# Optimization experiments

Measured on AMD Instinct MI355X. Metric: run time of the kernel, lower is better.

## Reference

```python
import jax, jax.numpy as jnp
import numpy as np

NUM_HEAD = 8
NUM_BOX = 4
K = 4                      # kernel_size
P = K * K                  # num_point
HEAD_DIM = 32
V_DIM = 256
Q_DIM = 256


def _kernel_indices():
    # even kernel: linspace(-K/2+0.5, K/2-0.5, K), stack (j, i) i.e. (x, y), /K
    idx = np.linspace(-K // 2 + 0.5, K // 2 - 0.5, K)
    i, j = np.meshgrid(idx, idx, indexing='ij')
    return jnp.asarray(np.stack([j, i], axis=-1).reshape(-1, 2) / K, dtype=jnp.float32)


def _bilinear(vm, gx, gy, Hf, Wf):
    # vm: [b,H,Hf*Wf,dh]; gx,gy: [b,H,M] normalized coords in [0,1]
    # grid_sample(2*g-1, align_corners=False, padding_mode='zeros') semantics
    x = gx * Wf - 0.5
    y = gy * Hf - 0.5
    x0 = jnp.floor(x)
    y0 = jnp.floor(y)
    wx1 = x - x0
    wy1 = y - y0

    def corner(xi, yi, w):
        inb = (xi >= 0) & (xi < Wf) & (yi >= 0) & (yi < Hf)
        xi_c = jnp.clip(xi, 0, Wf - 1).astype(jnp.int32)
        yi_c = jnp.clip(yi, 0, Hf - 1).astype(jnp.int32)
        v = jnp.take_along_axis(vm, (yi_c * Wf + xi_c)[..., None], axis=2)
        return v * (w * inb)[..., None]

    return (corner(x0, y0, (1 - wx1) * (1 - wy1))
            + corner(x0 + 1, y0, wx1 * (1 - wy1))
            + corner(x0, y0 + 1, (1 - wx1) * wy1)
            + corner(x0 + 1, y0 + 1, wx1 * wy1))


def _forward(query, value, Hf, Wf, v_mask, v_valid_ratios, ref_windows,
             box_w, box_b, attn_w, attn_b, vproj_w, vproj_b, oproj_w, oproj_b):
    b, l1, _ = query.shape
    l2 = value.shape[1]
    ki = _kernel_indices()  # [P,2]

    value = value @ vproj_w.T + vproj_b
    value = jnp.where(v_mask[..., None], 0.0, value)
    vm = value.reshape(b, l2, NUM_HEAD, HEAD_DIM).transpose(0, 2, 1, 3)  # [b,H,l2,dh]

    off = (query @ box_w.T + box_b).reshape(b, l1, NUM_HEAD, NUM_BOX, 4)
    ref = ref_windows[:, :, None, None, :]                   # [b,l1,1,1,4]
    ref_size = ref[..., jnp.array([2, 3, 2, 3])]
    boxes = ref + off / 8.0 * ref_size                       # [b,l1,H,B,4]
    center = boxes[..., None, :2]
    size = boxes[..., None, 2:]
    grid = center + ki * jax.nn.relu(size)                   # [b,l1,H,B,P,2]
    grid = grid * v_valid_ratios

    # attention weights: [b,l1,H,B,2,2] -> repeat_interleave -> [b,l1,H,B,K,K]
    aw = (query @ attn_w.T + attn_b).reshape(b, l1, NUM_HEAD, NUM_BOX, 2, 2)
    aw = jnp.repeat(jnp.repeat(aw, K // 2, axis=-1), K // 2, axis=-2)
    spatial_w = jax.nn.softmax(aw.reshape(b, l1, NUM_HEAD, NUM_BOX * P), axis=-1)
    level_w = jax.nn.softmax(aw, axis=3).reshape(b, l1, NUM_HEAD, NUM_BOX * P)

    # per-head bilinear sampling at all B*P points per query
    g = grid.transpose(0, 2, 1, 3, 4, 5).reshape(b, NUM_HEAD, -1, 2)  # [b,H,l1*B*P,2]
    sampled = _bilinear(vm, g[..., 0], g[..., 1], Hf, Wf)             # [b,H,M,dh]
    sampled = sampled.reshape(b, NUM_HEAD, l1, NUM_BOX * P, HEAD_DIM)

    out = jnp.einsum('bhlpd,blhp->blhd', sampled, spatial_w).reshape(b, l1, V_DIM)
    output = out @ oproj_w.T + oproj_b
    # mask branch: level softmax (over boxes) weighted aggregate, summed over points
    mout = jnp.einsum('bhlpd,blhp->blhd', sampled, level_w).reshape(b, l1, V_DIM)
    mask_output = mout @ oproj_w.T + oproj_b
    return output, mask_output, aw


def setup_inputs() -> dict:
    key = jax.random.key(0)
    ks = jax.random.split(key, 12)
    b, l1, Hf, Wf = 8, 300, 64, 64
    l2 = Hf * Wf
    d = Q_DIM
    return {
        'query': jax.random.normal(ks[0], (b, l1, d), jnp.float32),
        'value': jax.random.normal(ks[1], (b, l2, V_DIM), jnp.float32),
        'v_shape': np.array([[Hf, Wf]], dtype=np.int64),
        'v_mask': jnp.zeros((b, l2), dtype=bool),
        'v_start_index': np.array([0], dtype=np.int64),
        'v_valid_ratios': jnp.ones((b, 1, 1, 1, 1, 2), jnp.float32),
        'ref_windows': jax.random.uniform(ks[2], (b, l1, 4), jnp.float32, 0.05, 0.6),
        'box_w': 0.02 * jax.random.normal(ks[3], (NUM_BOX * NUM_HEAD * 4, d), jnp.float32),
        'box_b': jax.random.uniform(ks[4], (NUM_HEAD * NUM_BOX * 4,), jnp.float32),
        'attn_w': 0.02 * jax.random.normal(ks[5], (NUM_HEAD * NUM_BOX * 4, d), jnp.float32),
        'attn_b': 0.1 * jax.random.normal(ks[6], (NUM_HEAD * NUM_BOX * 4,), jnp.float32),
        'vproj_w': 0.05 * jax.random.normal(ks[7], (V_DIM, V_DIM), jnp.float32),
        'vproj_b': jnp.zeros((V_DIM,), jnp.float32),
        'oproj_w': 0.05 * jax.random.normal(ks[8], (d, V_DIM), jnp.float32),
        'oproj_b': jnp.zeros((d,), jnp.float32),
    }


def reference(query, value, v_shape, v_mask, v_start_index, v_valid_ratios, ref_windows,
              box_w, box_b, attn_w, attn_b, vproj_w, vproj_b, oproj_w, oproj_b):
    Hf, Wf = int(v_shape[0, 0]), int(v_shape[0, 1])  # single level, static shapes
    return _forward(query, value, Hf, Wf, v_mask, v_valid_ratios, ref_windows,
                    box_w, box_b, attn_w, attn_b, vproj_w, vproj_b, oproj_w, oproj_b)
```

## Files before the change

kernel.cpp:

```cpp
#include <hip/hip_runtime.h>
#include <cstddef>

#define NH   8
#define NB   4
#define HD   32
#define NPIX 4096
#define NBATCH 8
#define NL   300
#define D    256
#define NQ   (NBATCH * NL)
#define NR   (2 * NQ)

typedef __attribute__((ext_vector_type(4))) float  f32x4;
typedef __attribute__((ext_vector_type(8))) short  bf16x8;

__device__ __forceinline__ unsigned short f2bf(float f) {
    union { float f; unsigned u; } v; v.f = f;
    unsigned r = v.u + 0x7fffu + ((v.u >> 16) & 1u);
    return (unsigned short)(r >> 16);
}
__device__ __forceinline__ float bf2f(unsigned short u) {
    union { unsigned u; float f; } v; v.u = ((unsigned)u) << 16; return v.f;
}
__device__ __forceinline__ unsigned cvtpk(float lo, float hi) {
    unsigned r;
    asm("v_cvt_pk_bf16_f32 %0, %1, %2" : "=v"(r) : "v"(lo), "v"(hi));
    return r;
}
__device__ __forceinline__ bf16x8 pack8c(f32x4 a, f32x4 b) {
    union { unsigned u[4]; bf16x8 v; } r;
    r.u[0] = cvtpk(a[0], a[1]); r.u[1] = cvtpk(a[2], a[3]);
    r.u[2] = cvtpk(b[0], b[1]); r.u[3] = cvtpk(b[2], b[3]);
    return r.v;
}

__global__ __launch_bounds__(256)
void tow_kernel(const float* __restrict__ vproj_w, const float* __restrict__ oproj_w,
                unsigned short* __restrict__ wv, unsigned short* __restrict__ wo)
{
    const int i = blockIdx.x * 256 + threadIdx.x;
    const float* src = (i < 8192) ? vproj_w : oproj_w;
    unsigned short* dst = (i < 8192) ? wv : wo;
    const size_t off = (size_t)(i & 8191) * 8;
    f32x4 a = *(const f32x4*)(src + off);
    f32x4 b = *(const f32x4*)(src + off + 4);
    *(bf16x8*)(dst + off) = pack8c(a, b);
}

__global__ __launch_bounds__(256)
void fat_kernel(const float* __restrict__ value, const unsigned short* __restrict__ Wv,
                const float* __restrict__ vbias, const unsigned char* __restrict__ mask,
                unsigned short* __restrict__ vm,
                const float* __restrict__ query,
                const float* __restrict__ box_w, const float* __restrict__ box_b,
                const float* __restrict__ attn_w, const float* __restrict__ attn_b,
                float* __restrict__ bp, float* __restrict__ ap, float* __restrict__ awo)
{
    __shared__ float As[16][65];
    __shared__ float Bs[16][65];
    const int bid = blockIdx.x;
    const int tid = threadIdx.x;

    if (bid < 512) {
        const int lane = tid & 63, wid = tid >> 6;
        const int wm = wid >> 1, wn = wid & 1;
        const int row0 = bid * 64;
        const int l16 = lane & 15, lg = lane >> 4;

        f32x4 acc[2][8] = {};
        const float*          pa0 = value + (size_t)(row0 + wm * 32 + l16) * D + lg * 8;
        const unsigned short* pb0 = Wv    + (size_t)(wn * 128 + l16) * D + lg * 8;

        #pragma unroll
        for (int ks = 0; ks < 8; ++ks) {
            bf16x8 af[2], bfr[8];
            #pragma unroll
            for (int m = 0; m < 2; ++m) {
                const float* pa = pa0 + (size_t)m * 16 * D + ks * 32;
                af[m] = pack8c(*(const f32x4*)pa, *(const f32x4*)(pa + 4));
            }
            #pragma unroll
            for (int n = 0; n < 8; ++n)
                bfr[n] = *(const bf16x8*)(pb0 + (size_t)n * 16 * D + ks * 32);
            #pragma unroll
            for (int m = 0; m < 2; ++m)
                #pragma unroll
                for (int n = 0; n < 8; ++n)
                    acc[m][n] = __builtin_amdgcn_mfma_f32_16x16x32_bf16(af[m], bfr[n], acc[m][n], 0, 0, 0);
        }
        #pragma unroll
        for (int m = 0; m < 2; ++m) {
            #pragma unroll
            for (int r = 0; r < 4; ++r) {
                const int grow = row0 + wm * 32 + m * 16 + lg * 4 + r;
                const int bb = grow >> 12, pix = grow & (NPIX - 1);
                const float mf = (mask[grow] != 0) ? 0.f : 1.f;
                #pragma unroll
                for (int n = 0; n < 8; ++n) {
                    const int gcol = wn * 128 + n * 16 + l16;
                    const int h = gcol >> 5, dd = gcol & 31;
                    vm[((size_t)(bb * NH + h) * NPIX + pix) * HD + dd] =
                        f2bf(mf * (acc[m][n][r] + vbias[gcol]));
                }
            }
        }
    } else {
        const int pid = bid - 512;
        const int row0 = (pid % 38) * 64, col0 = (pid / 38) * 64;
        const int tr = tid >> 4, tc = tid & 15;
        float acc[4][4] = {};
        for (int k0 = 0; k0 < D; k0 += 16) {
            #pragma unroll
            for (int i = 0; i < 4; ++i) {
                int idx = tid + i * 256;
                int r = idx >> 4, kk = idx & 15;
                int qrow = min(row0 + r, NQ - 1);
                As[kk][r] = query[(size_t)qrow * D + k0 + kk];
                int c256 = col0 + r;
                const float* src = (c256 < 128) ? (box_w + (size_t)c256 * D)
                                                : (attn_w + (size_t)(c256 - 128) * D);
                Bs[kk][r] = src[k0 + kk];
            }
            __syncthreads();
            #pragma unroll
            for (int kk = 0; kk < 16; ++kk) {
                float a[4], bv[4];
                #pragma unroll
                for (int i = 0; i < 4; ++i) a[i] = As[kk][tr * 4 + i];
                #pragma unroll
                for (int j = 0; j < 4; ++j) bv[j] = Bs[kk][tc * 4 + j];
                #pragma unroll
                for (int i = 0; i < 4; ++i)
                    #pragma unroll
                    for (int j = 0; j < 4; ++j)
                        acc[i][j] += a[i] * bv[j];
            }
            __syncthreads();
        }
        #pragma unroll
        for (int i = 0; i < 4; ++i) {
            int q = row0 + tr * 4 + i;
            if (q >= NQ) continue;
            #pragma unroll
            for (int j = 0; j < 4; ++j) {
                int col = col0 + tc * 4 + j;
                if (col < 128) {
                    bp[(size_t)q * 128 + col] = acc[i][j] + box_b[col];
                } else {
                    int rc = col - 128;
                    float val = acc[i][j] + attn_b[rc];
                    ap[(size_t)q * 128 + rc] = val;
                    int h = rc >> 4, bx = (rc >> 2) & 3, rr = (rc >> 1) & 1, cc = rc & 1;
                    float* awq = awo + (size_t)q * 512 + (size_t)(h * NB + bx) * 16;
                    awq[(2 * rr + 0) * 4 + 2 * cc + 0] = val;
                    awq[(2 * rr + 0) * 4 + 2 * cc + 1] = val;
                    awq[(2 * rr + 1) * 4 + 2 * cc + 0] = val;
                    awq[(2 * rr + 1) * 4 + 2 * cc + 1] = val;
                }
            }
        }
    }
}

__global__ __launch_bounds__(256)
void sample_kernel(const unsigned short* __restrict__ vm, const float* __restrict__ bp,
                   const float* __restrict__ ap, const float* __restrict__ ref_windows,
                   const float* __restrict__ vratio, const int* __restrict__ vshape,
                   float* __restrict__ outp, float* __restrict__ moutp)
{
    __shared__ float sbp[128], sap[128], swh[128], lwh[128], sref4[4];
    __shared__ float4 boxdat[32];
    __shared__ int4   O4[512];
    __shared__ float4 W4[512];
    __shared__ float2 SL[512];
    const int blk = blockIdx.x, tid = threadIdx.x;
    const int bb = blk / NL;
    if (tid < 128) { sbp[tid] = bp[(size_t)blk * 128 + tid]; sap[tid] = ap[(size_t)blk * 128 + tid]; }
    if (tid < 4) sref4[tid] = ref_windows[(size_t)blk * 4 + tid];
    __syncthreads();
    const int Hf = vshape[0], Wf = vshape[1];
    const float Hff = (float)Hf, Wff = (float)Wf;
    const float vr0 = vratio[bb * 2 + 0], vr1 = vratio[bb * 2 + 1];

    if (tid < 128) {
        float a = sap[tid];
        float m = a;
        m = fmaxf(m, __shfl_xor(m, 1));
        m = fmaxf(m, __shfl_xor(m, 2));
        m = fmaxf(m, __shfl_xor(m, 4));
        m = fmaxf(m, __shfl_xor(m, 8));
        float e = expf(a - m);
        float ldv = e + __shfl_xor(e, 4);
        ldv += __shfl_xor(ldv, 8);
        float ss = ldv + __shfl_xor(ldv, 1);
        ss += __shfl_xor(ss, 2);
        swh[tid] = e / (4.f * ss);
        lwh[tid] = e / ldv;
    } else if (tid < 160) {
        int j = tid - 128;
        float o0 = sbp[j * 4 + 0], o1 = sbp[j * 4 + 1];
        float o2 = sbp[j * 4 + 2], o3 = sbp[j * 4 + 3];
        float cx = sref4[0] + o0 * 0.125f * sref4[2];
        float cy = sref4[1] + o1 * 0.125f * sref4[3];
        float rw = fmaxf(sref4[2] + o2 * 0.125f * sref4[2], 0.f);
        float rh = fmaxf(sref4[3] + o3 * 0.125f * sref4[3], 0.f);
        boxdat[j] = make_float4(cx, cy, rw, rh);
    }
    __syncthreads();

    const float kidx[4] = {-0.375f, -0.125f, 0.125f, 0.375f};
    #pragma unroll
    for (int pp = 0; pp < 2; ++pp) {
        const int p = tid + pp * 256;
        const float4 bd = boxdat[p >> 4];
        const int ii = (p >> 2) & 3, jj = p & 3;
        const float gy = (bd.y + kidx[ii] * bd.w) * vr1;
        const float gx = (bd.x + kidx[jj] * bd.z) * vr0;
        const float y = gy * Hff - 0.5f, x = gx * Wff - 0.5f;
        const float y0f = floorf(y), x0f = floorf(x);
        const int iy0 = (int)y0f, ix0 = (int)x0f;
        const float wy1 = y - y0f, wx1 = x - x0f;
        const float wy0 = 1.f - wy1, wx0 = 1.f - wx1;
        const bool y0in = (iy0 >= 0) & (iy0 < Hf);
        const bool y1in = (iy0 + 1 >= 0) & (iy0 + 1 < Hf);
        const bool x0in = (ix0 >= 0) & (ix0 < Wf);
        const bool x1in = (ix0 + 1 >= 0) & (ix0 + 1 < Wf);
        const int yc0 = min(max(iy0, 0), Hf - 1), yc1 = min(max(iy0 + 1, 0), Hf - 1);
        const int xc0 = min(max(ix0, 0), Wf - 1), xc1 = min(max(ix0 + 1, 0), Wf - 1);
        O4[p] = make_int4((yc0 * Wf + xc0) * HD, (yc0 * Wf + xc1) * HD,
                          (yc1 * Wf + xc0) * HD, (yc1 * Wf + xc1) * HD);
        W4[p] = make_float4((y0in & x0in) ? wy0 * wx0 : 0.f,
                            (y0in & x1in) ? wy0 * wx1 : 0.f,
                            (y1in & x0in) ? wy1 * wx0 : 0.f,
                            (y1in & x1in) ? wy1 * wx1 : 0.f);
        const int kpos = ((p >> 2) & 2) | ((p >> 1) & 1);
        const int hk = (p >> 6) * 16 + ((p >> 4) & 3) * 4 + kpos;
        SL[p] = make_float2(swh[hk], lwh[hk]);
    }
    __syncthreads();

    const int h = tid >> 5, dd = tid & 31;
    const unsigned short* base = vm + ((size_t)(bb * NH + h) * NPIX) * HD + dd;
    float acc = 0.f, accm = 0.f;
    #pragma unroll 4
    for (int t = 0; t < 64; ++t) {
        const int p = h * 64 + t;
        const int4 o = O4[p]; const float4 w = W4[p]; const float2 sl = SL[p];
        const float samp = bf2f(base[o.x]) * w.x + bf2f(base[o.y]) * w.y
                         + bf2f(base[o.z]) * w.z + bf2f(base[o.w]) * w.w;
        acc  += samp * sl.x;
        accm += samp * sl.y;
    }
    outp[(size_t)blk * 256 + tid]  = acc;
    moutp[(size_t)blk * 256 + tid] = accm;
}

__global__ __launch_bounds__(256)
void oproj_direct(const float* __restrict__ R, const unsigned short* __restrict__ Wo,
                  const float* __restrict__ bias, float* __restrict__ Out)
{
    const int tid  = threadIdx.x;
    const int lane = tid & 63, wid = tid >> 6;
    const int wm = wid >> 1, wn = wid & 1;
    const int row0 = blockIdx.x * 64;
    const int l16 = lane & 15, lg = lane >> 4;

    f32x4 acc[2][8] = {};
    const float*          pa0 = R  + (size_t)(row0 + wm * 32 + l16) * D + lg * 8;
    const unsigned short* pb0 = Wo + (size_t)(wn * 128 + l16) * D + lg * 8;

    #pragma unroll
    for (int ks = 0; ks < 8; ++ks) {
        bf16x8 af[2], bfr[8];
        #pragma unroll
        for (int m = 0; m < 2; ++m) {
            const float* pa = pa0 + (size_t)m * 16 * D + ks * 32;
            af[m] = pack8c(*(const f32x4*)pa, *(const f32x4*)(pa + 4));
        }
        #pragma unroll
        for (int n = 0; n < 8; ++n)
            bfr[n] = *(const bf16x8*)(pb0 + (size_t)n * 16 * D + ks * 32);
        #pragma unroll
        for (int m = 0; m < 2; ++m)
            #pragma unroll
            for (int n = 0; n < 8; ++n)
                acc[m][n] = __builtin_amdgcn_mfma_f32_16x16x32_bf16(af[m], bfr[n], acc[m][n], 0, 0, 0);
    }
    #pragma unroll
    for (int m = 0; m < 2; ++m) {
        #pragma unroll
        for (int r = 0; r < 4; ++r) {
            const int grow = row0 + wm * 32 + m * 16 + lg * 4 + r;
            #pragma unroll
            for (int n = 0; n < 8; ++n) {
                const int gcol = wn * 128 + n * 16 + l16;
                Out[(size_t)grow * D + gcol] = acc[m][n][r] + bias[gcol];
            }
        }
    }
}

extern "C" void kernel_launch(void* const* d_in, const int* in_sizes, int n_in,
                              void* d_out, int out_size, void* d_ws, size_t ws_size,
                              hipStream_t stream)
{
    const float* query        = (const float*)d_in[0];
    const float* value        = (const float*)d_in[1];
    const int*   vshape       = (const int*)d_in[2];
    const unsigned char* vmask= (const unsigned char*)d_in[3];
    const float* vratio       = (const float*)d_in[5];
    const float* refw         = (const float*)d_in[6];
    const float* box_w        = (const float*)d_in[7];
    const float* box_b        = (const float*)d_in[8];
    const float* attn_w       = (const float*)d_in[9];
    const float* attn_b       = (const float*)d_in[10];
    const float* vproj_w      = (const float*)d_in[11];
    const float* vproj_b      = (const float*)d_in[12];
    const float* oproj_w      = (const float*)d_in[13];
    const float* oproj_b      = (const float*)d_in[14];

    unsigned short* vm_b = (unsigned short*)d_ws;
    unsigned short* wv   = vm_b + 8388608;
    unsigned short* wo   = wv + 65536;
    float* bp = (float*)(wo + 65536);
    float* ap = bp + 307200;

    float* out1 = (float*)d_out;
    float* out2 = out1 + 614400;
    float* awo  = out2 + 614400;

    float* outp  = out1;
    float* moutp = out2;

    tow_kernel<<<64, 256, 0, stream>>>(vproj_w, oproj_w, wv, wo);
    fat_kernel<<<664, 256, 0, stream>>>(value, wv, vproj_b, vmask, vm_b,
                                        query, box_w, box_b, attn_w, attn_b, bp, ap, awo);
    sample_kernel<<<NQ, 256, 0, stream>>>(vm_b, bp, ap, refw, vratio, vshape, outp, moutp);
    oproj_direct<<<75, 256, 0, stream>>>(out1, wo, oproj_b, out1);
}
```

Measured before the change: 206.7 us.

## Stage GEMM operands in LDS with bf16 conversion and drop weight pre-conversion kernel

The value-projection and output-projection GEMMs now load fp32 tiles from global memory, convert them to bf16, and stage them in shared memory before the MFMA loops. Previously each wave read its operands straight from global memory. Operands are now reused across waves and the separate weight-conversion kernel launch is removed. The output projection moves to 128x256 tiles on 512-thread blocks, which halves the block count to 38. That may underuse the GPU's compute units, and the GEMMs now pay for extra barriers and shared-memory traffic.

```diff
diff --git a/kernel.cpp b/kernel.cpp
--- a/kernel.cpp
+++ b/kernel.cpp
@@ -35,20 +35,7 @@
 }
 
 __global__ __launch_bounds__(256)
-void tow_kernel(const float* __restrict__ vproj_w, const float* __restrict__ oproj_w,
-                unsigned short* __restrict__ wv, unsigned short* __restrict__ wo)
-{
-    const int i = blockIdx.x * 256 + threadIdx.x;
-    const float* src = (i < 8192) ? vproj_w : oproj_w;
-    unsigned short* dst = (i < 8192) ? wv : wo;
-    const size_t off = (size_t)(i & 8191) * 8;
-    f32x4 a = *(const f32x4*)(src + off);
-    f32x4 b = *(const f32x4*)(src + off + 4);
-    *(bf16x8*)(dst + off) = pack8c(a, b);
-}
-
-__global__ __launch_bounds__(256)
-void fat_kernel(const float* __restrict__ value, const unsigned short* __restrict__ Wv,
+void fat_kernel(const float* __restrict__ value, const float* __restrict__ Wvf,
                 const float* __restrict__ vbias, const unsigned char* __restrict__ mask,
                 unsigned short* __restrict__ vm,
                 const float* __restrict__ query,
@@ -56,48 +43,57 @@
                 const float* __restrict__ attn_w, const float* __restrict__ attn_b,
                 float* __restrict__ bp, float* __restrict__ ap, float* __restrict__ awo)
 {
-    __shared__ float As[16][65];
-    __shared__ float Bs[16][65];
+    __shared__ __align__(16) short As[128][72];
+    __shared__ __align__(16) short Bs[128][72];
     const int bid = blockIdx.x;
     const int tid = threadIdx.x;
 
     if (bid < 512) {
+        const int mt = bid >> 1, nt = bid & 1;
+        const int row0 = mt * 128, col0 = nt * 128;
         const int lane = tid & 63, wid = tid >> 6;
         const int wm = wid >> 1, wn = wid & 1;
-        const int row0 = bid * 64;
         const int l16 = lane & 15, lg = lane >> 4;
 
-        f32x4 acc[2][8] = {};
-        const float*          pa0 = value + (size_t)(row0 + wm * 32 + l16) * D + lg * 8;
-        const unsigned short* pb0 = Wv    + (size_t)(wn * 128 + l16) * D + lg * 8;
-
-        #pragma unroll
-        for (int ks = 0; ks < 8; ++ks) {
-            bf16x8 af[2], bfr[8];
-            #pragma unroll
-            for (int m = 0; m < 2; ++m) {
-                const float* pa = pa0 + (size_t)m * 16 * D + ks * 32;
-                af[m] = pack8c(*(const f32x4*)pa, *(const f32x4*)(pa + 4));
-            }
-            #pragma unroll
-            for (int n = 0; n < 8; ++n)
-                bfr[n] = *(const bf16x8*)(pb0 + (size_t)n * 16 * D + ks * 32);
-            #pragma unroll
-            for (int m = 0; m < 2; ++m)
-                #pragma unroll
-                for (int n = 0; n < 8; ++n)
-                    acc[m][n] = __builtin_amdgcn_mfma_f32_16x16x32_bf16(af[m], bfr[n], acc[m][n], 0, 0, 0);
-        }
-        #pragma unroll
-        for (int m = 0; m < 2; ++m) {
+        f32x4 acc[4][4] = {};
+        for (int k0 = 0; k0 < D; k0 += 64) {
+            #pragma unroll
+            for (int i = 0; i < 4; ++i) {
+                const int t = tid + i * 256;
+                const int r = t >> 3, c8 = (t & 7) * 8;
+                const float* p = value + (size_t)(row0 + r) * D + k0 + c8;
+                *(bf16x8*)&As[r][c8] = pack8c(*(const f32x4*)p, *(const f32x4*)(p + 4));
+                const float* q = Wvf + (size_t)(col0 + r) * D + k0 + c8;
+                *(bf16x8*)&Bs[r][c8] = pack8c(*(const f32x4*)q, *(const f32x4*)(q + 4));
+            }
+            __syncthreads();
+            #pragma unroll
+            for (int kk = 0; kk < 2; ++kk) {
+                bf16x8 af[4], bfr[4];
+                #pragma unroll
+                for (int m = 0; m < 4; ++m)
+                    af[m] = *(const bf16x8*)&As[wm * 64 + m * 16 + l16][kk * 32 + lg * 8];
+                #pragma unroll
+                for (int n = 0; n < 4; ++n)
+                    bfr[n] = *(const bf16x8*)&Bs[wn * 64 + n * 16 + l16][kk * 32 + lg * 8];
+                #pragma unroll
+                for (int m = 0; m < 4; ++m)
+                    #pragma unroll
+                    for (int n = 0; n < 4; ++n)
+                        acc[m][n] = __builtin_amdgcn_mfma_f32_16x16x32_bf16(af[m], bfr[n], acc[m][n], 0, 0, 0);
+            }
+            __syncthreads();
+        }
+        #pragma unroll
+        for (int m = 0; m < 4; ++m) {
             #pragma unroll
             for (int r = 0; r < 4; ++r) {
-                const int grow = row0 + wm * 32 + m * 16 + lg * 4 + r;
+                const int grow = row0 + wm * 64 + m * 16 + lg * 4 + r;
                 const int bb = grow >> 12, pix = grow & (NPIX - 1);
                 const float mf = (mask[grow] != 0) ? 0.f : 1.f;
                 #pragma unroll
-                for (int n = 0; n < 8; ++n) {
-                    const int gcol = wn * 128 + n * 16 + l16;
+                for (int n = 0; n < 4; ++n) {
+                    const int gcol = col0 + wn * 64 + n * 16 + l16;
                     const int h = gcol >> 5, dd = gcol & 31;
                     vm[((size_t)(bb * NH + h) * NPIX + pix) * HD + dd] =
                         f2bf(mf * (acc[m][n][r] + vbias[gcol]));
@@ -105,6 +101,8 @@
             }
         }
     } else {
+        float (*Asf)[65] = (float (*)[65])&As[0][0];
+        float (*Bsf)[65] = (float (*)[65])&Bs[0][0];
         const int pid = bid - 512;
         const int row0 = (pid % 38) * 64, col0 = (pid / 38) * 64;
         const int tr = tid >> 4, tc = tid & 15;
@@ -115,20 +113,20 @@
                 int idx = tid + i * 256;
                 int r = idx >> 4, kk = idx & 15;
                 int qrow = min(row0 + r, NQ - 1);
-                As[kk][r] = query[(size_t)qrow * D + k0 + kk];
+                Asf[kk][r] = query[(size_t)qrow * D + k0 + kk];
                 int c256 = col0 + r;
                 const float* src = (c256 < 128) ? (box_w + (size_t)c256 * D)
                                                 : (attn_w + (size_t)(c256 - 128) * D);
-                Bs[kk][r] = src[k0 + kk];
+                Bsf[kk][r] = src[k0 + kk];
             }
             __syncthreads();
             #pragma unroll
             for (int kk = 0; kk < 16; ++kk) {
                 float a[4], bv[4];
                 #pragma unroll
-                for (int i = 0; i < 4; ++i) a[i] = As[kk][tr * 4 + i];
-                #pragma unroll
-                for (int j = 0; j < 4; ++j) bv[j] = Bs[kk][tc * 4 + j];
+                for (int i = 0; i < 4; ++i) a[i] = Asf[kk][tr * 4 + i];
+                #pragma unroll
+                for (int j = 0; j < 4; ++j) bv[j] = Bsf[kk][tc * 4 + j];
                 #pragma unroll
                 for (int i = 0; i < 4; ++i)
                     #pragma unroll
@@ -255,45 +253,62 @@
     moutp[(size_t)blk * 256 + tid] = accm;
 }
 
-__global__ __launch_bounds__(256)
-void oproj_direct(const float* __restrict__ R, const unsigned short* __restrict__ Wo,
-                  const float* __restrict__ bias, float* __restrict__ Out)
+__global__ __launch_bounds__(512)
+void oproj_lds(const float* __restrict__ R, const float* __restrict__ Wof,
+               const float* __restrict__ bias, float* __restrict__ Out)
 {
+    __shared__ __align__(16) short As[128][72];
+    __shared__ __align__(16) short Bs[256][72];
     const int tid  = threadIdx.x;
     const int lane = tid & 63, wid = tid >> 6;
-    const int wm = wid >> 1, wn = wid & 1;
-    const int row0 = blockIdx.x * 64;
+    const int wm = wid >> 2, wn = wid & 3;
+    const int row0 = blockIdx.x * 128;
     const int l16 = lane & 15, lg = lane >> 4;
 
-    f32x4 acc[2][8] = {};
-    const float*          pa0 = R  + (size_t)(row0 + wm * 32 + l16) * D + lg * 8;
-    const unsigned short* pb0 = Wo + (size_t)(wn * 128 + l16) * D + lg * 8;
-
+    f32x4 acc[4][4] = {};
+    for (int k0 = 0; k0 < D; k0 += 64) {
+        #pragma unroll
+        for (int i = 0; i < 2; ++i) {
+            const int t = tid + i * 512;
+            const int r = t >> 3, c8 = (t & 7) * 8;
+            const int arow = min(row0 + r, NR - 1);
+            const float* p = R + (size_t)arow * D + k0 + c8;
+            *(bf16x8*)&As[r][c8] = pack8c(*(const f32x4*)p, *(const f32x4*)(p + 4));
+        }
+        #pragma unroll
+        for (int i = 0; i < 4; ++i) {
+            const int t = tid + i * 512;
+            const int r = t >> 3, c8 = (t & 7) * 8;
+            const float* q = Wof + (size_t)r * D + k0 + c8;
+            *(bf16x8*)&Bs[r][c8] = pack8c(*(const f32x4*)q, *(const f32x4*)(q + 4));
+        }
+        __syncthreads();
+        #pragma unroll
+        for (int kk = 0; kk < 2; ++kk) {
+            bf16x8 af[4], bfr[4];
+            #pragma unroll
+            for (int m = 0; m < 4; ++m)
+                af[m] = *(const bf16x8*)&As[wm * 64 + m * 16 + l16][kk * 32 + lg * 8];
+            #pragma unroll
+            for (int n = 0; n < 4; ++n)
+                bfr[n] = *(const bf16x8*)&Bs[wn * 64 + n * 16 + l16][kk * 32 + lg * 8];
+            #pragma unroll
+            for (int m = 0; m < 4; ++m)
+                #pragma unroll
+                for (int n = 0; n < 4; ++n)
+                    acc[m][n] = __builtin_amdgcn_mfma_f32_16x16x32_bf16(af[m], bfr[n], acc[m][n], 0, 0, 0);
+        }
+        __syncthreads();
+    }
     #pragma unroll
-    for (int ks = 0; ks < 8; ++ks) {
-        bf16x8 af[2], bfr[8];
-        #pragma unroll
-        for (int m = 0; m < 2; ++m) {
-            const float* pa = pa0 + (size_t)m * 16 * D + ks * 32;
-            af[m] = pack8c(*(const f32x4*)pa, *(const f32x4*)(pa + 4));
-        }
-        #pragma unroll
-        for (int n = 0; n < 8; ++n)
-            bfr[n] = *(const bf16x8*)(pb0 + (size_t)n * 16 * D + ks * 32);
-        #pragma unroll
-        for (int m = 0; m < 2; ++m)
-            #pragma unroll
-            for (int n = 0; n < 8; ++n)
-                acc[m][n] = __builtin_amdgcn_mfma_f32_16x16x32_bf16(af[m], bfr[n], acc[m][n], 0, 0, 0);
-    }
-    #pragma unroll
-    for (int m = 0; m < 2; ++m) {
+    for (int m = 0; m < 4; ++m) {
         #pragma unroll
         for (int r = 0; r < 4; ++r) {
-            const int grow = row0 + wm * 32 + m * 16 + lg * 4 + r;
-            #pragma unroll
-            for (int n = 0; n < 8; ++n) {
-                const int gcol = wn * 128 + n * 16 + l16;
+            const int grow = row0 + wm * 64 + m * 16 + lg * 4 + r;
+            if (grow >= NR) continue;
+            #pragma unroll
+            for (int n = 0; n < 4; ++n) {
+                const int gcol = wn * 64 + n * 16 + l16;
                 Out[(size_t)grow * D + gcol] = acc[m][n][r] + bias[gcol];
             }
         }
@@ -320,9 +335,7 @@
     const float* oproj_b      = (const float*)d_in[14];
 
     unsigned short* vm_b = (unsigned short*)d_ws;
-    unsigned short* wv   = vm_b + 8388608;
-    unsigned short* wo   = wv + 65536;
-    float* bp = (float*)(wo + 65536);
+    float* bp = (float*)(vm_b + 8388608);
     float* ap = bp + 307200;
 
     float* out1 = (float*)d_out;
@@ -332,9 +345,8 @@
     float* outp  = out1;
     float* moutp = out2;
 
-    tow_kernel<<<64, 256, 0, stream>>>(vproj_w, oproj_w, wv, wo);
-    fat_kernel<<<664, 256, 0, stream>>>(value, wv, vproj_b, vmask, vm_b,
+    fat_kernel<<<664, 256, 0, stream>>>(value, vproj_w, vproj_b, vmask, vm_b,
                                         query, box_w, box_b, attn_w, attn_b, bp, ap, awo);
     sample_kernel<<<NQ, 256, 0, stream>>>(vm_b, bp, ap, refw, vratio, vshape, outp, moutp);
-    oproj_direct<<<75, 256, 0, stream>>>(out1, wo, oproj_b, out1);
-}
+    oproj_lds<<<38, 512, 0, stream>>>(out1, oproj_w, oproj_b, out1);
+}
```

Result: faster. 198.0 us (-4.2%).

## Fuse output projection into sampling kernel and tile value projection through LDS

Applied to the files above, without the earlier changes.

The output projection is folded into the sampling kernel: each block keeps its two 256-wide sampled vectors in shared memory and runs a per-thread fp32 GEMV against the fp32 oproj weights. This removes the separate oproj GEMM launch and the global round trip of the intermediate. The value projection becomes its own 512-thread MFMA kernel that stages bf16-converted value and weight tiles in LDS with register prefetch, which drops the weight-conversion pre-kernel. The query projection is split out as a separate 2D-grid kernel, and sample blocks are remapped to interleave batches. The cost is that every sampling block re-reads the full fp32 oproj weight with strided per-thread row loads, does that GEMV without tensor cores, and the two projection GEMMs no longer share one launch.

```diff
diff --git a/kernel.cpp b/kernel.cpp
--- a/kernel.cpp
+++ b/kernel.cpp
@@ -9,7 +9,6 @@
 #define NL   300
 #define D    256
 #define NQ   (NBATCH * NL)
-#define NR   (2 * NQ)
 
 typedef __attribute__((ext_vector_type(4))) float  f32x4;
 typedef __attribute__((ext_vector_type(8))) short  bf16x8;
@@ -34,129 +33,137 @@
     return r.v;
 }
 
+__global__ __launch_bounds__(512, 4)
+void vproj_kernel(const float* __restrict__ value, const float* __restrict__ Wvf,
+                  const float* __restrict__ vbias, const unsigned char* __restrict__ mask,
+                  unsigned short* __restrict__ vm)
+{
+    __shared__ __align__(16) short As[64][72];
+    __shared__ __align__(16) short Bs[256][72];
+    const int tid  = threadIdx.x;
+    const int lane = tid & 63, wid = tid >> 6;
+    const int wm = wid >> 2, wn = wid & 3;
+    const int row0 = blockIdx.x * 64;
+    const int l16 = lane & 15, lg = lane >> 4;
+
+    const int sr = tid >> 3, sc8 = (tid & 7) * 8;
+
+    f32x4 acc[2][4] = {};
+    f32x4 pA[2], pB[8];
+
+    auto LOADK = [&](int k0) {
+        const float* p = value + (size_t)(row0 + sr) * D + k0 + sc8;
+        pA[0] = *(const f32x4*)p; pA[1] = *(const f32x4*)(p + 4);
+        #pragma unroll
+        for (int i = 0; i < 4; ++i) {
+            const float* q = Wvf + (size_t)(sr + i * 64) * D + k0 + sc8;
+            pB[2 * i] = *(const f32x4*)q; pB[2 * i + 1] = *(const f32x4*)(q + 4);
+        }
+    };
+
+    LOADK(0);
+    #pragma unroll
+    for (int ks = 0; ks < 4; ++ks) {
+        *(bf16x8*)&As[sr][sc8] = pack8c(pA[0], pA[1]);
+        #pragma unroll
+        for (int i = 0; i < 4; ++i)
+            *(bf16x8*)&Bs[sr + i * 64][sc8] = pack8c(pB[2 * i], pB[2 * i + 1]);
+        __syncthreads();
+        if (ks < 3) LOADK((ks + 1) * 64);
+        #pragma unroll
+        for (int kk = 0; kk < 2; ++kk) {
+            bf16x8 af[2], bfr[4];
+            #pragma unroll
+            for (int m = 0; m < 2; ++m)
+                af[m] = *(const bf16x8*)&As[wm * 32 + m * 16 + l16][kk * 32 + lg * 8];
+            #pragma unroll
+            for (int n = 0; n < 4; ++n)
+                bfr[n] = *(const bf16x8*)&Bs[wn * 64 + n * 16 + l16][kk * 32 + lg * 8];
+            #pragma unroll
+            for (int m = 0; m < 2; ++m)
+                #pragma unroll
+                for (int n = 0; n < 4; ++n)
+                    acc[m][n] = __builtin_amdgcn_mfma_f32_16x16x32_bf16(af[m], bfr[n], acc[m][n], 0, 0, 0);
+        }
+        __syncthreads();
+    }
+    #pragma unroll
+    for (int m = 0; m < 2; ++m) {
+        #pragma unroll
+        for (int r = 0; r < 4; ++r) {
+            const int grow = row0 + wm * 32 + m * 16 + lg * 4 + r;
+            const int bb = grow >> 12, pix = grow & (NPIX - 1);
+            const float mf = (mask[grow] != 0) ? 0.f : 1.f;
+            #pragma unroll
+            for (int n = 0; n < 4; ++n) {
+                const int gcol = wn * 64 + n * 16 + l16;
+                const int h = gcol >> 5, dd = gcol & 31;
+                vm[((size_t)(bb * NH + h) * NPIX + pix) * HD + dd] =
+                    f2bf(mf * (acc[m][n][r] + vbias[gcol]));
+            }
+        }
+    }
+}
+
 __global__ __launch_bounds__(256)
-void tow_kernel(const float* __restrict__ vproj_w, const float* __restrict__ oproj_w,
-                unsigned short* __restrict__ wv, unsigned short* __restrict__ wo)
-{
-    const int i = blockIdx.x * 256 + threadIdx.x;
-    const float* src = (i < 8192) ? vproj_w : oproj_w;
-    unsigned short* dst = (i < 8192) ? wv : wo;
-    const size_t off = (size_t)(i & 8191) * 8;
-    f32x4 a = *(const f32x4*)(src + off);
-    f32x4 b = *(const f32x4*)(src + off + 4);
-    *(bf16x8*)(dst + off) = pack8c(a, b);
-}
-
-__global__ __launch_bounds__(256)
-void fat_kernel(const float* __restrict__ value, const unsigned short* __restrict__ Wv,
-                const float* __restrict__ vbias, const unsigned char* __restrict__ mask,
-                unsigned short* __restrict__ vm,
-                const float* __restrict__ query,
-                const float* __restrict__ box_w, const float* __restrict__ box_b,
-                const float* __restrict__ attn_w, const float* __restrict__ attn_b,
-                float* __restrict__ bp, float* __restrict__ ap, float* __restrict__ awo)
+void proj_kernel(const float* __restrict__ query,
+                 const float* __restrict__ box_w, const float* __restrict__ box_b,
+                 const float* __restrict__ attn_w, const float* __restrict__ attn_b,
+                 float* __restrict__ bp, float* __restrict__ ap, float* __restrict__ awo)
 {
     __shared__ float As[16][65];
     __shared__ float Bs[16][65];
-    const int bid = blockIdx.x;
     const int tid = threadIdx.x;
-
-    if (bid < 512) {
-        const int lane = tid & 63, wid = tid >> 6;
-        const int wm = wid >> 1, wn = wid & 1;
-        const int row0 = bid * 64;
-        const int l16 = lane & 15, lg = lane >> 4;
-
-        f32x4 acc[2][8] = {};
-        const float*          pa0 = value + (size_t)(row0 + wm * 32 + l16) * D + lg * 8;
-        const unsigned short* pb0 = Wv    + (size_t)(wn * 128 + l16) * D + lg * 8;
-
-        #pragma unroll
-        for (int ks = 0; ks < 8; ++ks) {
-            bf16x8 af[2], bfr[8];
-            #pragma unroll
-            for (int m = 0; m < 2; ++m) {
-                const float* pa = pa0 + (size_t)m * 16 * D + ks * 32;
-                af[m] = pack8c(*(const f32x4*)pa, *(const f32x4*)(pa + 4));
-            }
-            #pragma unroll
-            for (int n = 0; n < 8; ++n)
-                bfr[n] = *(const bf16x8*)(pb0 + (size_t)n * 16 * D + ks * 32);
-            #pragma unroll
-            for (int m = 0; m < 2; ++m)
+    const int tr = tid >> 4, tc = tid & 15;
+    float acc[4][4] = {};
+    const int row0 = blockIdx.x * 64, col0 = blockIdx.y * 64;
+    for (int k0 = 0; k0 < D; k0 += 16) {
+        #pragma unroll
+        for (int i = 0; i < 4; ++i) {
+            int idx = tid + i * 256;
+            int r = idx >> 4, kk = idx & 15;
+            int qrow = min(row0 + r, NQ - 1);
+            As[kk][r] = query[(size_t)qrow * D + k0 + kk];
+            int c256 = col0 + r;
+            const float* src = (c256 < 128) ? (box_w + (size_t)c256 * D)
+                                            : (attn_w + (size_t)(c256 - 128) * D);
+            Bs[kk][r] = src[k0 + kk];
+        }
+        __syncthreads();
+        #pragma unroll
+        for (int kk = 0; kk < 16; ++kk) {
+            float a[4], bv[4];
+            #pragma unroll
+            for (int i = 0; i < 4; ++i) a[i] = As[kk][tr * 4 + i];
+            #pragma unroll
+            for (int j = 0; j < 4; ++j) bv[j] = Bs[kk][tc * 4 + j];
+            #pragma unroll
+            for (int i = 0; i < 4; ++i)
                 #pragma unroll
-                for (int n = 0; n < 8; ++n)
-                    acc[m][n] = __builtin_amdgcn_mfma_f32_16x16x32_bf16(af[m], bfr[n], acc[m][n], 0, 0, 0);
-        }
-        #pragma unroll
-        for (int m = 0; m < 2; ++m) {
-            #pragma unroll
-            for (int r = 0; r < 4; ++r) {
-                const int grow = row0 + wm * 32 + m * 16 + lg * 4 + r;
-                const int bb = grow >> 12, pix = grow & (NPIX - 1);
-                const float mf = (mask[grow] != 0) ? 0.f : 1.f;
-                #pragma unroll
-                for (int n = 0; n < 8; ++n) {
-                    const int gcol = wn * 128 + n * 16 + l16;
-                    const int h = gcol >> 5, dd = gcol & 31;
-                    vm[((size_t)(bb * NH + h) * NPIX + pix) * HD + dd] =
-                        f2bf(mf * (acc[m][n][r] + vbias[gcol]));
-                }
-            }
-        }
-    } else {
-        const int pid = bid - 512;
-        const int row0 = (pid % 38) * 64, col0 = (pid / 38) * 64;
-        const int tr = tid >> 4, tc = tid & 15;
-        float acc[4][4] = {};
-        for (int k0 = 0; k0 < D; k0 += 16) {
-            #pragma unroll
-            for (int i = 0; i < 4; ++i) {
-                int idx = tid + i * 256;
-                int r = idx >> 4, kk = idx & 15;
-                int qrow = min(row0 + r, NQ - 1);
-                As[kk][r] = query[(size_t)qrow * D + k0 + kk];
-                int c256 = col0 + r;
-                const float* src = (c256 < 128) ? (box_w + (size_t)c256 * D)
-                                                : (attn_w + (size_t)(c256 - 128) * D);
-                Bs[kk][r] = src[k0 + kk];
-            }
-            __syncthreads();
-            #pragma unroll
-            for (int kk = 0; kk < 16; ++kk) {
-                float a[4], bv[4];
-                #pragma unroll
-                for (int i = 0; i < 4; ++i) a[i] = As[kk][tr * 4 + i];
-                #pragma unroll
-                for (int j = 0; j < 4; ++j) bv[j] = Bs[kk][tc * 4 + j];
-                #pragma unroll
-                for (int i = 0; i < 4; ++i)
-                    #pragma unroll
-                    for (int j = 0; j < 4; ++j)
-                        acc[i][j] += a[i] * bv[j];
-            }
-            __syncthreads();
-        }
-        #pragma unroll
-        for (int i = 0; i < 4; ++i) {
-            int q = row0 + tr * 4 + i;
-            if (q >= NQ) continue;
-            #pragma unroll
-            for (int j = 0; j < 4; ++j) {
-                int col = col0 + tc * 4 + j;
-                if (col < 128) {
-                    bp[(size_t)q * 128 + col] = acc[i][j] + box_b[col];
-                } else {
-                    int rc = col - 128;
-                    float val = acc[i][j] + attn_b[rc];
-                    ap[(size_t)q * 128 + rc] = val;
-                    int h = rc >> 4, bx = (rc >> 2) & 3, rr = (rc >> 1) & 1, cc = rc & 1;
-                    float* awq = awo + (size_t)q * 512 + (size_t)(h * NB + bx) * 16;
-                    awq[(2 * rr + 0) * 4 + 2 * cc + 0] = val;
-                    awq[(2 * rr + 0) * 4 + 2 * cc + 1] = val;
-                    awq[(2 * rr + 1) * 4 + 2 * cc + 0] = val;
-                    awq[(2 * rr + 1) * 4 + 2 * cc + 1] = val;
-                }
+                for (int j = 0; j < 4; ++j)
+                    acc[i][j] += a[i] * bv[j];
+        }
+        __syncthreads();
+    }
+    #pragma unroll
+    for (int i = 0; i < 4; ++i) {
+        int q = row0 + tr * 4 + i;
+        if (q >= NQ) continue;
+        #pragma unroll
+        for (int j = 0; j < 4; ++j) {
+            int col = col0 + tc * 4 + j;
+            if (col < 128) {
+                bp[(size_t)q * 128 + col] = acc[i][j] + box_b[col];
+            } else {
+                int rc = col - 128;
+                float val = acc[i][j] + attn_b[rc];
+                ap[(size_t)q * 128 + rc] = val;
+                int h = rc >> 4, bx = (rc >> 2) & 3, rr = (rc >> 1) & 1, cc = rc & 1;
+                float* awq = awo + (size_t)q * 512 + (size_t)(h * NB + bx) * 16;
+                awq[(2 * rr + 0) * 4 + 2 * cc + 0] = val;
+                awq[(2 * rr + 0) * 4 + 2 * cc + 1] = val;
+                awq[(2 * rr + 1) * 4 + 2 * cc + 0] = val;
+                awq[(2 * rr + 1) * 4 + 2 * cc + 1] = val;
             }
         }
     }
@@ -166,14 +173,17 @@
 void sample_kernel(const unsigned short* __restrict__ vm, const float* __restrict__ bp,
                    const float* __restrict__ ap, const float* __restrict__ ref_windows,
                    const float* __restrict__ vratio, const int* __restrict__ vshape,
-                   float* __restrict__ outp, float* __restrict__ moutp)
+                   const float* __restrict__ oproj_w, const float* __restrict__ oproj_b,
+                   float* __restrict__ out1, float* __restrict__ out2)
 {
     __shared__ float sbp[128], sap[128], swh[128], lwh[128], sref4[4];
     __shared__ float4 boxdat[32];
     __shared__ int4   O4[512];
     __shared__ float4 W4[512];
     __shared__ float2 SL[512];
-    const int blk = blockIdx.x, tid = threadIdx.x;
+    __shared__ __align__(16) float r1s[256], r2s[256];
+    const int bid = blockIdx.x, tid = threadIdx.x;
+    const int blk = (bid & 7) * NL + (bid >> 3);
     const int bb = blk / NL;
     if (tid < 128) { sbp[tid] = bp[(size_t)blk * 128 + tid]; sap[tid] = ap[(size_t)blk * 128 + tid]; }
     if (tid < 4) sref4[tid] = ref_windows[(size_t)blk * 4 + tid];
@@ -239,65 +249,36 @@
     }
     __syncthreads();
 
-    const int h = tid >> 5, dd = tid & 31;
-    const unsigned short* base = vm + ((size_t)(bb * NH + h) * NPIX) * HD + dd;
-    float acc = 0.f, accm = 0.f;
-    #pragma unroll 4
-    for (int t = 0; t < 64; ++t) {
-        const int p = h * 64 + t;
-        const int4 o = O4[p]; const float4 w = W4[p]; const float2 sl = SL[p];
-        const float samp = bf2f(base[o.x]) * w.x + bf2f(base[o.y]) * w.y
-                         + bf2f(base[o.z]) * w.z + bf2f(base[o.w]) * w.w;
-        acc  += samp * sl.x;
-        accm += samp * sl.y;
-    }
-    outp[(size_t)blk * 256 + tid]  = acc;
-    moutp[(size_t)blk * 256 + tid] = accm;
-}
-
-__global__ __launch_bounds__(256)
-void oproj_direct(const float* __restrict__ R, const unsigned short* __restrict__ Wo,
-                  const float* __restrict__ bias, float* __restrict__ Out)
-{
-    const int tid  = threadIdx.x;
-    const int lane = tid & 63, wid = tid >> 6;
-    const int wm = wid >> 1, wn = wid & 1;
-    const int row0 = blockIdx.x * 64;
-    const int l16 = lane & 15, lg = lane >> 4;
-
-    f32x4 acc[2][8] = {};
-    const float*          pa0 = R  + (size_t)(row0 + wm * 32 + l16) * D + lg * 8;
-    const unsigned short* pb0 = Wo + (size_t)(wn * 128 + l16) * D + lg * 8;
-
-    #pragma unroll
-    for (int ks = 0; ks < 8; ++ks) {
-        bf16x8 af[2], bfr[8];
-        #pragma unroll
-        for (int m = 0; m < 2; ++m) {
-            const float* pa = pa0 + (size_t)m * 16 * D + ks * 32;
-            af[m] = pack8c(*(const f32x4*)pa, *(const f32x4*)(pa + 4));
-        }
-        #pragma unroll
-        for (int n = 0; n < 8; ++n)
-            bfr[n] = *(const bf16x8*)(pb0 + (size_t)n * 16 * D + ks * 32);
-        #pragma unroll
-        for (int m = 0; m < 2; ++m)
-            #pragma unroll
-            for (int n = 0; n < 8; ++n)
-                acc[m][n] = __builtin_amdgcn_mfma_f32_16x16x32_bf16(af[m], bfr[n], acc[m][n], 0, 0, 0);
-    }
-    #pragma unroll
-    for (int m = 0; m < 2; ++m) {
-        #pragma unroll
-        for (int r = 0; r < 4; ++r) {
-            const int grow = row0 + wm * 32 + m * 16 + lg * 4 + r;
-            #pragma unroll
-            for (int n = 0; n < 8; ++n) {
-                const int gcol = wn * 128 + n * 16 + l16;
-                Out[(size_t)grow * D + gcol] = acc[m][n][r] + bias[gcol];
-            }
-        }
-    }
+    {
+        const int h = tid >> 5, dd = tid & 31;
+        const unsigned short* base = vm + ((size_t)(bb * NH + h) * NPIX) * HD + dd;
+        float acc = 0.f, accm = 0.f;
+        #pragma unroll 4
+        for (int t = 0; t < 64; ++t) {
+            const int p = h * 64 + t;
+            const int4 o = O4[p]; const float4 w = W4[p]; const float2 sl = SL[p];
+            const float samp = bf2f(base[o.x]) * w.x + bf2f(base[o.y]) * w.y
+                             + bf2f(base[o.z]) * w.z + bf2f(base[o.w]) * w.w;
+            acc  += samp * sl.x;
+            accm += samp * sl.y;
+        }
+        r1s[tid] = acc;
+        r2s[tid] = accm;
+    }
+    __syncthreads();
+
+    float a1 = oproj_b[tid], a2 = a1;
+    const float* wr = oproj_w + (size_t)tid * 256;
+    #pragma unroll 8
+    for (int v = 0; v < 256; v += 4) {
+        const f32x4 wv = *(const f32x4*)(wr + v);
+        const f32x4 x1 = *(const f32x4*)&r1s[v];
+        const f32x4 x2 = *(const f32x4*)&r2s[v];
+        a1 += wv[0] * x1[0] + wv[1] * x1[1] + wv[2] * x1[2] + wv[3] * x1[3];
+        a2 += wv[0] * x2[0] + wv[1] * x2[1] + wv[2] * x2[2] + wv[3] * x2[3];
+    }
+    out1[(size_t)blk * 256 + tid] = a1;
+    out2[(size_t)blk * 256 + tid] = a2;
 }
 
 extern "C" void kernel_launch(void* const* d_in, const int* in_sizes, int n_in,
@@ -320,21 +301,15 @@
     const float* oproj_b      = (const float*)d_in[14];
 
     unsigned short* vm_b = (unsigned short*)d_ws;
-    unsigned short* wv   = vm_b + 8388608;
-    unsigned short* wo   = wv + 65536;
-    float* bp = (float*)(wo + 65536);
+    float* bp = (float*)(vm_b + 8388608);
     float* ap = bp + 307200;
 
     float* out1 = (float*)d_out;
     float* out2 = out1 + 614400;
     float* awo  = out2 + 614400;
 
-    float* outp  = out1;
-    float* moutp = out2;
-
-    tow_kernel<<<64, 256, 0, stream>>>(vproj_w, oproj_w, wv, wo);
-    fat_kernel<<<664, 256, 0, stream>>>(value, wv, vproj_b, vmask, vm_b,
-                                        query, box_w, box_b, attn_w, attn_b, bp, ap, awo);
-    sample_kernel<<<NQ, 256, 0, stream>>>(vm_b, bp, ap, refw, vratio, vshape, outp, moutp);
-    oproj_direct<<<75, 256, 0, stream>>>(out1, wo, oproj_b, out1);
-}
+    vproj_kernel<<<512, 512, 0, stream>>>(value, vproj_w, vproj_b, vmask, vm_b);
+    proj_kernel<<<dim3(38, 4), 256, 0, stream>>>(query, box_w, box_b, attn_w, attn_b, bp, ap, awo);
+    sample_kernel<<<NQ, 256, 0, stream>>>(vm_b, bp, ap, refw, vratio, vshape,
+                                          oproj_w, oproj_b, out1, out2);
+}
```

After: 243.0 us. 1.18x slower.
